# Performance work log

Measured on AMD Instinct MI355X. Metric: run time of the kernel, lower is better.

The kernel has to match this reference:

```python
import jax, jax.numpy as jnp
import numpy as np

# Build the three 3x3x3 Sobel kernels once, stacked as [O=3, I=1, 3,3,3]
def _sobel_kernels():
    kx = np.array([[[-1,0,1],[-2,0,2],[-1,0,1]],
                   [[-2,0,2],[-4,0,4],[-2,0,2]],
                   [[-1,0,1],[-2,0,2],[-1,0,1]]], dtype=np.float32)
    ky = np.array([[[-1,-2,-1],[0,0,0],[1,2,1]],
                   [[-2,-4,-2],[0,0,0],[2,4,2]],
                   [[-1,-2,-1],[0,0,0],[1,2,1]]], dtype=np.float32)
    kz = np.array([[[-1,-2,-1],[-2,-4,-2],[-1,-2,-1]],
                   [[0,0,0],[0,0,0],[0,0,0]],
                   [[1,2,1],[2,4,2],[1,2,1]]], dtype=np.float32)
    return jnp.asarray(np.stack([kx, ky, kz])[:, None])  # [3,1,3,3,3]

_K = _sobel_kernels()
_EPS = 1e-08

def _grad_mag(x):
    # x: [B,1,D,H,W] -> fused conv producing all 3 gradient channels at once
    g = jax.lax.conv_general_dilated(
        x, _K, window_strides=(1, 1, 1), padding='SAME',
        dimension_numbers=('NCDHW', 'OIDHW', 'NCDHW'))  # [B,3,D,H,W]
    return jnp.sqrt(jnp.sum(g * g, axis=1, keepdims=True) + _EPS)  # [B,1,D,H,W]


def setup_inputs() -> dict:
    key = jax.random.key(0)
    k1, k2 = jax.random.split(key)
    shape = (2, 1, 160, 192, 160)
    pred = jax.random.normal(k1, shape, dtype=jnp.float32)
    target = jax.random.normal(k2, shape, dtype=jnp.float32)
    return {"pred": pred, "target": target}


def reference(pred, target):
    pg = _grad_mag(pred)
    tg = _grad_mag(target)
    # penalty='l1' -> F.l1_loss mean reduction
    return jnp.mean(jnp.abs(pg - tg))
```

## Files before the change

### kernel.cpp

```cpp
#include <hip/hip_runtime.h>

namespace {
constexpr int Wd = 160, Hd = 192, Dd = 160, Bd = 2;
constexpr int HW = Hd * Wd;
constexpr int THREADS = 256;
constexpr int ROWS_OUT = 12;
constexpr int ROWS_LDS = 14;
constexpr int RS = 164;
constexpr int STRIPS = 40;
constexpr int CTHREADS = 240;
constexpr int TASKS = 2 * ROWS_LDS * STRIPS;
constexpr int NSLOT = 5;
constexpr int DCHUNK = 10;
constexpr int NCHUNK = Dd / DCHUNK;
constexpr int RGROUPS = Hd / ROWS_OUT;
constexpr float EPS = 1e-8f;
}

using v4f = __attribute__((ext_vector_type(4))) float;
using v4h = __attribute__((ext_vector_type(4))) _Float16;

__device__ __forceinline__ float dpp_up1(float v) {
  return __int_as_float(__builtin_amdgcn_update_dpp(
      0, __float_as_int(v), 0x138, 0xF, 0xF, true));
}
__device__ __forceinline__ float dpp_dn1(float v) {
  return __int_as_float(__builtin_amdgcn_update_dpp(
      0, __float_as_int(v), 0x130, 0xF, 0xF, true));
}

__global__ __launch_bounds__(THREADS) void sobel_loss_kernel(
    const float* __restrict__ pred, const float* __restrict__ targ,
    float* __restrict__ out) {
  __shared__ __align__(16) _Float16 lsw[2][ROWS_LDS][RS];
  __shared__ __align__(16) _Float16 ldw[2][ROWS_LDS][RS];
  const int tid = threadIdx.x;
  const int lane = tid & 63;
  const int h0 = blockIdx.x * ROWS_OUT;
  const int d0 = blockIdx.y * DCHUNK;
  const size_t volOff = (size_t)blockIdx.z * Dd * HW;
  const float* pb = pred + volOff;
  const float* tb = targ + volOff;

  const float* gs[NSLOT];
  _Float16* psw[NSLOT];
  _Float16* pdw[NSLOT];
  bool sok[NSLOT], rok[NSLOT], zL[NSLOT], zR[NSLOT], pL[NSLOT], pR[NSLOT];
#pragma unroll
  for (int u = 0; u < NSLOT; ++u) {
    const int i = tid + 256 * u;
    const bool ok = (i < TASKS);
    const int ic = ok ? i : 0;
    const int t_ = ic / (ROWS_LDS * STRIPS);
    const int rem = ic - t_ * (ROWS_LDS * STRIPS);
    const int r8 = rem / STRIPS, s = rem - r8 * STRIPS;
    const int hh = h0 - 1 + r8;
    const bool rv = ok && ((unsigned)hh < (unsigned)Hd);
    sok[u] = ok;
    rok[u] = rv;
    zL[u] = (s == 0);
    zR[u] = (s == STRIPS - 1);
    pL[u] = ok && (lane == 0) && (s != 0);
    pR[u] = ok && (lane == 63) && (s != STRIPS - 1);
    gs[u] = (t_ ? tb : pb) + (size_t)(rv ? hh : 0) * Wd + s * 4;
    psw[u] = &lsw[t_][r8][s * 4];
    pdw[u] = &ldw[t_][r8][s * 4];
  }

  float4 m[NSLOT];
  float hl[NSLOT], hr[NSLOT];
  auto GLOAD = [&](int d) {
    const bool dok = (unsigned)d < (unsigned)Dd;
    const size_t so = (size_t)d * HW;
#pragma unroll
    for (int u = 0; u < NSLOT; ++u) {
      float4 v = make_float4(0.f, 0.f, 0.f, 0.f);
      float a = 0.f, b = 0.f;
      if (dok && rok[u]) {
        v = *reinterpret_cast<const float4*>(gs[u] + so);
        if (pL[u]) a = gs[u][so - 1];
        if (pR[u]) b = gs[u][so + 4];
      }
      m[u] = v; hl[u] = a; hr[u] = b;
    }
  };

  auto STAGE = [&]() {
#pragma unroll
    for (int u = 0; u < NSLOT; ++u) {
      float xl = dpp_up1(m[u].w);
      float xr = dpp_dn1(m[u].x);
      if (zL[u]) xl = 0.f;
      if (pL[u]) xl = hl[u];
      if (zR[u]) xr = 0.f;
      if (pR[u]) xr = hr[u];
      const float x0 = xl, x1 = m[u].x, x2 = m[u].y, x3 = m[u].z,
                  x4 = m[u].w, x5 = xr;
      v4f swf, dwf;
      swf[0] = fmaf(2.f, x1, x0 + x2);  dwf[0] = x2 - x0;
      swf[1] = fmaf(2.f, x2, x1 + x3);  dwf[1] = x3 - x1;
      swf[2] = fmaf(2.f, x3, x2 + x4);  dwf[2] = x4 - x2;
      swf[3] = fmaf(2.f, x4, x3 + x5);  dwf[3] = x5 - x3;
      if (sok[u]) {
        *reinterpret_cast<v4h*>(psw[u]) = __builtin_convertvector(swf, v4h);
        *reinterpret_cast<v4h*>(pdw[u]) = __builtin_convertvector(dwf, v4h);
      }
    }
  };

  const int cr = tid / STRIPS;
  const int cs4 = (tid - cr * STRIPS) * 4;
  const bool is_c = (tid < CTHREADS);

  v4h A[3][2][2], B[3][2][2], C[3][2][2];
  const _Float16 h2 = (_Float16)2.0f;

  auto HCONV = [&](int slot) {
#pragma unroll
    for (int hf = 0; hf < 2; ++hf) {
      const int r = cr + hf * 6;
#pragma unroll
      for (int t_ = 0; t_ < 2; ++t_) {
        const v4h sm = *reinterpret_cast<const v4h*>(&lsw[t_][r][cs4]);
        const v4h s0 = *reinterpret_cast<const v4h*>(&lsw[t_][r + 1][cs4]);
        const v4h sp = *reinterpret_cast<const v4h*>(&lsw[t_][r + 2][cs4]);
        const v4h dm = *reinterpret_cast<const v4h*>(&ldw[t_][r][cs4]);
        const v4h dd = *reinterpret_cast<const v4h*>(&ldw[t_][r + 1][cs4]);
        const v4h dp = *reinterpret_cast<const v4h*>(&ldw[t_][r + 2][cs4]);
        A[slot][t_][hf] = s0 * h2 + (sm + sp);
        B[slot][t_][hf] = dd * h2 + (dm + dp);
        C[slot][t_][hf] = sp - sm;
      }
    }
  };

  v4f accv = {0.f, 0.f, 0.f, 0.f};

  auto EMITF = [&](int i0, int i1, int i2) {
#pragma unroll
    for (int hf = 0; hf < 2; ++hf) {
      const v4h gx0 = B[i1][0][hf] * h2 + (B[i0][0][hf] + B[i2][0][hf]);
      const v4h gy0 = C[i1][0][hf] * h2 + (C[i0][0][hf] + C[i2][0][hf]);
      const v4h gz0 = A[i2][0][hf] - A[i0][0][hf];
      const v4h q0h = gx0 * gx0 + gy0 * gy0 + gz0 * gz0;
      const v4h gx1 = B[i1][1][hf] * h2 + (B[i0][1][hf] + B[i2][1][hf]);
      const v4h gy1 = C[i1][1][hf] * h2 + (C[i0][1][hf] + C[i2][1][hf]);
      const v4h gz1 = A[i2][1][hf] - A[i0][1][hf];
      const v4h q1h = gx1 * gx1 + gy1 * gy1 + gz1 * gz1;
      const v4f q0 = __builtin_convertvector(q0h, v4f) + EPS;
      const v4f q1 = __builtin_convertvector(q1h, v4f) + EPS;
      v4f dd_;
#pragma unroll
      for (int j = 0; j < 4; ++j)
        dd_[j] = __builtin_amdgcn_sqrtf(q0[j]) - __builtin_amdgcn_sqrtf(q1[j]);
#pragma unroll
      for (int j = 0; j < 4; ++j) dd_[j] = fabsf(dd_[j]);
      accv += dd_;
    }
  };

  GLOAD(d0 - 1);
  STAGE(); GLOAD(d0); __syncthreads();
  if (is_c) HCONV(0);
  __syncthreads();
  STAGE(); GLOAD(d0 + 1); __syncthreads();
  if (is_c) HCONV(1);
  __syncthreads();

#pragma unroll
  for (int k = 0; k < DCHUNK; ++k) {
    STAGE();
    if (k < DCHUNK - 1) GLOAD(d0 + 2 + k);
    __syncthreads();
    const int i0 = k % 3, i1 = (k + 1) % 3, i2 = (k + 2) % 3;
    if (is_c) {
      HCONV(i2);
      EMITF(i0, i1, i2);
    }
    __syncthreads();
  }

  float sred = accv[0] + accv[1] + accv[2] + accv[3];
#pragma unroll
  for (int off = 32; off > 0; off >>= 1) sred += __shfl_down(sred, off, 64);
  __shared__ float wsum[THREADS / 64];
  const int wid = tid >> 6;
  if (lane == 0) wsum[wid] = sred;
  __syncthreads();
  if (tid == 0) {
    float t = 0.f;
#pragma unroll
    for (int i = 0; i < THREADS / 64; ++i) t += wsum[i];
    atomicAdd(out, t * (1.0f / (float)((size_t)Bd * Dd * Hd * Wd)));
  }
}

extern "C" void kernel_launch(void* const* d_in, const int* in_sizes, int n_in,
                              void* d_out, int out_size, void* d_ws, size_t ws_size,
                              hipStream_t stream) {
  const float* pred = (const float*)d_in[0];
  const float* targ = (const float*)d_in[1];
  float* out = (float*)d_out;
  (void)in_sizes; (void)n_in; (void)out_size; (void)d_ws; (void)ws_size;

  hipMemsetAsync(out, 0, sizeof(float), stream);
  dim3 grid(RGROUPS, NCHUNK, Bd);
  sobel_loss_kernel<<<grid, THREADS, 0, stream>>>(pred, targ, out);
}
```

Before: 33.84 us.

## Process two depth slices per barrier with double-buffered LDS staging

Doubles the LDS staging buffers and register prefetch sets so two depth slices are loaded, staged and convolved per pair of barriers. This halves the number of __syncthreads in the depth loop and keeps twice as many global loads in flight. In exchange it doubles LDS usage and raises register pressure, which may reduce occupancy.

Measured after the change: 35.51 us. 4.9% more time.

```diff
diff --git a/kernel.cpp b/kernel.cpp
--- a/kernel.cpp
+++ b/kernel.cpp
@@ -14,6 +14,7 @@
 constexpr int DCHUNK = 10;
 constexpr int NCHUNK = Dd / DCHUNK;
 constexpr int RGROUPS = Hd / ROWS_OUT;
+constexpr int BUFH = 2 * ROWS_LDS * RS;
 constexpr float EPS = 1e-8f;
 }
 
@@ -32,8 +33,8 @@
 __global__ __launch_bounds__(THREADS) void sobel_loss_kernel(
     const float* __restrict__ pred, const float* __restrict__ targ,
     float* __restrict__ out) {
-  __shared__ __align__(16) _Float16 lsw[2][ROWS_LDS][RS];
-  __shared__ __align__(16) _Float16 ldw[2][ROWS_LDS][RS];
+  __shared__ __align__(16) _Float16 lsw[2][2][ROWS_LDS][RS];
+  __shared__ __align__(16) _Float16 ldw[2][2][ROWS_LDS][RS];
   const int tid = threadIdx.x;
   const int lane = tid & 63;
   const int h0 = blockIdx.x * ROWS_OUT;
@@ -63,13 +64,15 @@
     pL[u] = ok && (lane == 0) && (s != 0);
     pR[u] = ok && (lane == 63) && (s != STRIPS - 1);
     gs[u] = (t_ ? tb : pb) + (size_t)(rv ? hh : 0) * Wd + s * 4;
-    psw[u] = &lsw[t_][r8][s * 4];
-    pdw[u] = &ldw[t_][r8][s * 4];
+    psw[u] = &lsw[0][t_][r8][s * 4];
+    pdw[u] = &ldw[0][t_][r8][s * 4];
   }
 
-  float4 m[NSLOT];
-  float hl[NSLOT], hr[NSLOT];
-  auto GLOAD = [&](int d) {
+  float4 mA[NSLOT], mB[NSLOT];
+  float hlA[NSLOT], hrA[NSLOT], hlB[NSLOT], hrB[NSLOT];
+
+  auto GLOADto = [&](int d, float4 (&m)[NSLOT], float (&hl)[NSLOT],
+                     float (&hr)[NSLOT]) {
     const bool dok = (unsigned)d < (unsigned)Dd;
     const size_t so = (size_t)d * HW;
 #pragma unroll
@@ -85,7 +88,8 @@
     }
   };
 
-  auto STAGE = [&]() {
+  auto STAGEfrom = [&](int b, const float4 (&m)[NSLOT],
+                       const float (&hl)[NSLOT], const float (&hr)[NSLOT]) {
 #pragma unroll
     for (int u = 0; u < NSLOT; ++u) {
       float xl = dpp_up1(m[u].w);
@@ -102,8 +106,10 @@
       swf[2] = fmaf(2.f, x3, x2 + x4);  dwf[2] = x4 - x2;
       swf[3] = fmaf(2.f, x4, x3 + x5);  dwf[3] = x5 - x3;
       if (sok[u]) {
-        *reinterpret_cast<v4h*>(psw[u]) = __builtin_convertvector(swf, v4h);
-        *reinterpret_cast<v4h*>(pdw[u]) = __builtin_convertvector(dwf, v4h);
+        *reinterpret_cast<v4h*>(psw[u] + b * BUFH) =
+            __builtin_convertvector(swf, v4h);
+        *reinterpret_cast<v4h*>(pdw[u] + b * BUFH) =
+            __builtin_convertvector(dwf, v4h);
       }
     }
   };
@@ -115,18 +121,18 @@
   v4h A[3][2][2], B[3][2][2], C[3][2][2];
   const _Float16 h2 = (_Float16)2.0f;
 
-  auto HCONV = [&](int slot) {
+  auto HCONV = [&](int slot, int b) {
 #pragma unroll
     for (int hf = 0; hf < 2; ++hf) {
       const int r = cr + hf * 6;
 #pragma unroll
       for (int t_ = 0; t_ < 2; ++t_) {
-        const v4h sm = *reinterpret_cast<const v4h*>(&lsw[t_][r][cs4]);
-        const v4h s0 = *reinterpret_cast<const v4h*>(&lsw[t_][r + 1][cs4]);
-        const v4h sp = *reinterpret_cast<const v4h*>(&lsw[t_][r + 2][cs4]);
-        const v4h dm = *reinterpret_cast<const v4h*>(&ldw[t_][r][cs4]);
-        const v4h dd = *reinterpret_cast<const v4h*>(&ldw[t_][r + 1][cs4]);
-        const v4h dp = *reinterpret_cast<const v4h*>(&ldw[t_][r + 2][cs4]);
+        const v4h sm = *reinterpret_cast<const v4h*>(&lsw[b][t_][r][cs4]);
+        const v4h s0 = *reinterpret_cast<const v4h*>(&lsw[b][t_][r + 1][cs4]);
+        const v4h sp = *reinterpret_cast<const v4h*>(&lsw[b][t_][r + 2][cs4]);
+        const v4h dm = *reinterpret_cast<const v4h*>(&ldw[b][t_][r][cs4]);
+        const v4h dd = *reinterpret_cast<const v4h*>(&ldw[b][t_][r + 1][cs4]);
+        const v4h dp = *reinterpret_cast<const v4h*>(&ldw[b][t_][r + 2][cs4]);
         A[slot][t_][hf] = s0 * h2 + (sm + sp);
         B[slot][t_][hf] = dd * h2 + (dm + dp);
         C[slot][t_][hf] = sp - sm;
@@ -159,23 +165,32 @@
     }
   };
 
-  GLOAD(d0 - 1);
-  STAGE(); GLOAD(d0); __syncthreads();
-  if (is_c) HCONV(0);
+  GLOADto(d0 - 1, mA, hlA, hrA);
+  GLOADto(d0,     mB, hlB, hrB);
+  STAGEfrom(0, mA, hlA, hrA);
+  STAGEfrom(1, mB, hlB, hrB);
+  GLOADto(d0 + 1, mA, hlA, hrA);
+  GLOADto(d0 + 2, mB, hlB, hrB);
   __syncthreads();
-  STAGE(); GLOAD(d0 + 1); __syncthreads();
-  if (is_c) HCONV(1);
+  if (is_c) { HCONV(0, 0); HCONV(1, 1); }
   __syncthreads();
 
 #pragma unroll
-  for (int k = 0; k < DCHUNK; ++k) {
-    STAGE();
-    if (k < DCHUNK - 1) GLOAD(d0 + 2 + k);
+  for (int j = 1; j <= DCHUNK / 2; ++j) {
+    STAGEfrom(0, mA, hlA, hrA);
+    STAGEfrom(1, mB, hlB, hrB);
+    if (j < DCHUNK / 2) {
+      GLOADto(d0 + 1 + 2 * j, mA, hlA, hrA);
+      GLOADto(d0 + 2 + 2 * j, mB, hlB, hrB);
+    }
     __syncthreads();
-    const int i0 = k % 3, i1 = (k + 1) % 3, i2 = (k + 2) % 3;
     if (is_c) {
-      HCONV(i2);
-      EMITF(i0, i1, i2);
+      const int na = 2 * j;
+      HCONV(na % 3, 0);
+      EMITF((na + 1) % 3, (na + 2) % 3, na % 3);
+      const int nb = 2 * j + 1;
+      HCONV(nb % 3, 1);
+      EMITF((nb + 1) % 3, (nb + 2) % 3, nb % 3);
     }
     __syncthreads();
   }
```
